# Kernel optimization log

Measured on AMD Instinct MI355X. Metric: run time of the kernel, lower is better.

The kernel has to match this reference:

```python
import jax, jax.numpy as jnp
import numpy as np

B, D_IN, D_OUT, M = 4096, 1024, 1024, 16
GAMMA = 2.0


def setup_inputs() -> dict:
    key = jax.random.key(0)
    ks = jax.random.split(key, 5)
    scale_in = 1.0 / np.sqrt(D_IN)
    return {
        "x": jax.random.normal(ks[0], (B, D_IN), dtype=jnp.float32),
        "W": jax.random.normal(ks[1], (M, D_IN, D_OUT), dtype=jnp.float32) * scale_in,
        "b": jax.random.normal(ks[2], (M, D_OUT), dtype=jnp.float32) * 0.01,
        "Wg": jax.random.normal(ks[3], (D_IN, M), dtype=jnp.float32) * scale_in,
        "bg": jax.random.normal(ks[4], (M,), dtype=jnp.float32) * 0.01,
    }


def reference(x, W, b, Wg, bg):
    # Gate: linear -> pow(gamma) -> normalize by row sum -> relu
    gu = x @ Wg + bg                                   # [B, M]
    gp = jnp.power(gu, GAMMA)                          # gamma = 2.0
    gates = jax.nn.relu(gp / jnp.sum(gp, axis=1, keepdims=True))  # [B, M]
    # M dense expert modules: relu(x @ W_m + b_m), gated and summed (AdditionSublayer)
    h = jax.nn.relu(jnp.einsum("bi,mio->bmo", x, W) + b)          # [B, M, D_OUT]
    return jnp.einsum("bm,bmo->bo", gates, h)                     # [B, D_OUT]
```

## Files before the change

### kernel.cpp

```cpp
#include <hip/hip_runtime.h>

typedef unsigned short u16;
typedef __attribute__((ext_vector_type(4))) float f32x4;
typedef __attribute__((ext_vector_type(8))) short bf16x8;
typedef __attribute__((ext_vector_type(4))) unsigned short u16x4;

#define NT 128

__device__ __forceinline__ u16 f2bf(float f) {
  union { float f; unsigned u; } v; v.f = f;
  unsigned r = v.u + 0x7FFFu + ((v.u >> 16) & 1u);
  return (u16)(r >> 16);
}

__device__ __forceinline__ f32x4 zero4() {
  f32x4 z; z.x = 0.f; z.y = 0.f; z.z = 0.f; z.w = 0.f; return z;
}

__global__ __launch_bounds__(256) void k_cvt_x(const float* __restrict__ x, u16* __restrict__ xb) {
  int i = blockIdx.x * 256 + threadIdx.x;
  f32x4 v = ((const f32x4*)x)[i];
  u16x4 o;
  o.x = f2bf(v.x); o.y = f2bf(v.y); o.z = f2bf(v.z); o.w = f2bf(v.w);
  ((u16x4*)xb)[i] = o;
}

__global__ __launch_bounds__(256) void k_tw(const float* __restrict__ W, u16* __restrict__ wt) {
  __shared__ float t[64][65];
  int bid = blockIdx.x;
  int e = bid >> 8, rem = bid & 255, kt = rem >> 4, nt = rem & 15;
  int tid = threadIdx.x;
  int c = tid & 63, r0 = tid >> 6;
  const float* src = W + (size_t)e * 1048576 + (size_t)(kt * 64) * 1024 + nt * 64;
  #pragma unroll
  for (int p = 0; p < 16; ++p) {
    int r = r0 + p * 4;
    t[r][c] = src[r * 1024 + c];
  }
  __syncthreads();
  u16* dst = wt + (size_t)e * 1048576 + (size_t)(nt * 64) * 1024 + kt * 64;
  #pragma unroll
  for (int p = 0; p < 16; ++p) {
    int r2 = r0 + p * 4;
    dst[r2 * 1024 + c] = f2bf(t[c][r2]);
  }
}

__global__ __launch_bounds__(256) void k_gates(const float* __restrict__ x, const float* __restrict__ Wg,
                                               const float* __restrict__ bg, float* __restrict__ gates) {
  int wid = threadIdx.x >> 6, lane = threadIdx.x & 63;
  int b = blockIdx.x * 4 + wid;
  const float* xr = x + (size_t)b * 1024;
  float acc[16];
  #pragma unroll
  for (int m = 0; m < 16; ++m) acc[m] = 0.f;
  for (int i = lane; i < 1024; i += 64) {
    float xv = xr[i];
    const f32x4* wg = (const f32x4*)(Wg + (size_t)i * 16);
    #pragma unroll
    for (int q = 0; q < 4; ++q) {
      f32x4 w = wg[q];
      acc[q*4+0] += xv * w.x; acc[q*4+1] += xv * w.y;
      acc[q*4+2] += xv * w.z; acc[q*4+3] += xv * w.w;
    }
  }
  #pragma unroll
  for (int m = 0; m < 16; ++m) {
    #pragma unroll
    for (int off = 32; off > 0; off >>= 1)
      acc[m] += __shfl_xor(acc[m], off, 64);
  }
  float tot = 0.f, gp[16];
  #pragma unroll
  for (int m = 0; m < 16; ++m) { float gu = acc[m] + bg[m]; gp[m] = gu * gu; tot += gp[m]; }
  float inv = 1.f / tot;
  if (lane == 0) {
    #pragma unroll
    for (int m = 0; m < 16; ++m) gates[(size_t)b * 16 + m] = gp[m] * inv;
  }
}

#define GLL(srcaddr, ldsaddr) \
  __builtin_amdgcn_global_load_lds((const __attribute__((address_space(1))) void*)(srcaddr), \
                                   (__attribute__((address_space(3))) void*)(ldsaddr), 16, 0, 0)

#define MFMA16() do { \
  acc[0][0] = __builtin_amdgcn_mfma_f32_16x16x32_bf16(af0, bfr0, acc[0][0], 0,0,0); \
  acc[0][1] = __builtin_amdgcn_mfma_f32_16x16x32_bf16(af0, bfr1, acc[0][1], 0,0,0); \
  acc[0][2] = __builtin_amdgcn_mfma_f32_16x16x32_bf16(af0, bfr2, acc[0][2], 0,0,0); \
  acc[0][3] = __builtin_amdgcn_mfma_f32_16x16x32_bf16(af0, bfr3, acc[0][3], 0,0,0); \
  acc[1][0] = __builtin_amdgcn_mfma_f32_16x16x32_bf16(af1, bfr0, acc[1][0], 0,0,0); \
  acc[1][1] = __builtin_amdgcn_mfma_f32_16x16x32_bf16(af1, bfr1, acc[1][1], 0,0,0); \
  acc[1][2] = __builtin_amdgcn_mfma_f32_16x16x32_bf16(af1, bfr2, acc[1][2], 0,0,0); \
  acc[1][3] = __builtin_amdgcn_mfma_f32_16x16x32_bf16(af1, bfr3, acc[1][3], 0,0,0); \
  acc[2][0] = __builtin_amdgcn_mfma_f32_16x16x32_bf16(af2, bfr0, acc[2][0], 0,0,0); \
  acc[2][1] = __builtin_amdgcn_mfma_f32_16x16x32_bf16(af2, bfr1, acc[2][1], 0,0,0); \
  acc[2][2] = __builtin_amdgcn_mfma_f32_16x16x32_bf16(af2, bfr2, acc[2][2], 0,0,0); \
  acc[2][3] = __builtin_amdgcn_mfma_f32_16x16x32_bf16(af2, bfr3, acc[2][3], 0,0,0); \
  acc[3][0] = __builtin_amdgcn_mfma_f32_16x16x32_bf16(af3, bfr0, acc[3][0], 0,0,0); \
  acc[3][1] = __builtin_amdgcn_mfma_f32_16x16x32_bf16(af3, bfr1, acc[3][1], 0,0,0); \
  acc[3][2] = __builtin_amdgcn_mfma_f32_16x16x32_bf16(af3, bfr2, acc[3][2], 0,0,0); \
  acc[3][3] = __builtin_amdgcn_mfma_f32_16x16x32_bf16(af3, bfr3, acc[3][3], 0,0,0); \
} while (0)

__global__ __launch_bounds__(512, 2)
void k_moe(const u16* __restrict__ xb, const u16* __restrict__ wt,
           const float* __restrict__ gates, const float* __restrict__ bias,
           float* __restrict__ out0, float* __restrict__ p1out) {
  __shared__ __align__(16) u16 sA[3 * 8192];
  __shared__ __align__(16) u16 sB[3 * 16384];
  __shared__ float lgat[1024];
  __shared__ float lbias[2048];

  int tid = threadIdx.x;
  int bid = blockIdx.x;
  int swz = (bid & 7) * 32 + (bid >> 3);
  int btile = swz & 31;
  int pnl = swz >> 5;
  int grp = pnl >> 2;
  int ntile = pnl & 3;
  int brow0 = btile * 128;
  int ncol0 = ntile * 256;
  int mb = grp * 8;

  int wid = tid >> 6, lane = tid & 63;
  int wm = wid >> 2, wn = wid & 3;
  int lrow = lane & 15, lk = lane >> 4;
  int sw = lrow & 7;

  const u16* asrc = xb + (size_t)brow0 * 1024;
  const u16* bsrc = wt + (size_t)mb * 1048576 + (size_t)ncol0 * 1024;

  int r0a = tid >> 3, s0a = tid & 7;
  int r1a = (512 + tid) >> 3, s1a = tid & 7;
  int sia0 = r0a * 1024 + (s0a ^ (r0a & 7)) * 8;
  int sia1 = r1a * 1024 + (s1a ^ (r1a & 7)) * 8;
  int lda0 = (wid * 64) * 8;
  int lda1 = (512 + wid * 64) * 8;
  int sib0 = sia0, sib1 = sia1;
  int r2b = (1024 + tid) >> 3;
  int r3b = (1536 + tid) >> 3;
  int sib2 = r2b * 1024 + ((tid & 7) ^ (r2b & 7)) * 8;
  int sib3 = r3b * 1024 + ((tid & 7) ^ (r3b & 7)) * 8;
  int ldb0 = lda0, ldb1 = lda1;
  int ldb2 = (1024 + wid * 64) * 8;
  int ldb3 = (1536 + wid * 64) * 8;

  int baseA = (wm * 64 + lrow) * 64;
  int baseB = (wn * 64 + lrow) * 64;
  int pa0 = baseA + ((0 + lk) ^ sw) * 8;
  int pa1 = baseA + ((4 + lk) ^ sw) * 8;
  int pb0 = baseB + ((0 + lk) ^ sw) * 8;
  int pb1 = baseB + ((4 + lk) ^ sw) * 8;

  f32x4 acc[4][4], oacc[4][4];
  #pragma unroll
  for (int i = 0; i < 4; ++i)
    #pragma unroll
    for (int j = 0; j < 4; ++j) { acc[i][j] = zero4(); oacc[i][j] = zero4(); }

  #pragma unroll
  for (int i = 0; i < 2; ++i) {
    int idx = i * 512 + tid;
    lgat[idx] = gates[(size_t)(brow0 + (idx & 127)) * 16 + mb + (idx >> 7)];
  }
  #pragma unroll
  for (int i = 0; i < 4; ++i) {
    int idx = i * 512 + tid;
    lbias[idx] = bias[(size_t)(mb + (idx >> 8)) * 1024 + ncol0 + (idx & 255)];
  }
  u16 *a0 = sA, *a1 = sA + 8192, *a2 = sA + 16384;
  u16 *b0 = sB, *b1 = sB + 16384, *b2 = sB + 32768;
  GLL(asrc + sia0, a0 + lda0); GLL(asrc + sia1, a0 + lda1);
  GLL(bsrc + sib0, b0 + ldb0); GLL(bsrc + sib1, b0 + ldb1);
  GLL(bsrc + sib2, b0 + ldb2); GLL(bsrc + sib3, b0 + ldb3);
  GLL(asrc + 64 + sia0, a1 + lda0); GLL(asrc + 64 + sia1, a1 + lda1);
  GLL(bsrc + 64 + sib0, b1 + ldb0); GLL(bsrc + 64 + sib1, b1 + ldb1);
  GLL(bsrc + 64 + sib2, b1 + ldb2); GLL(bsrc + 64 + sib3, b1 + ldb3);
  __syncthreads();

  for (int t = 0; t < NT; ++t) {
    int t2 = t + 2;
    const u16* sa2 = asrc + (t2 & 15) * 64;
    const u16* sb2 = bsrc + (size_t)(t2 >> 4) * 1048576 + (t2 & 15) * 64;
    bool pf = (t2 < NT);
    bf16x8 bfr0, bfr1, bfr2, bfr3, af0, af1, af2, af3;

    af0  = *(const bf16x8*)&a0[pa0];
    af1  = *(const bf16x8*)&a0[pa0 + 1024];
    af2  = *(const bf16x8*)&a0[pa0 + 2048];
    af3  = *(const bf16x8*)&a0[pa0 + 3072];
    bfr0 = *(const bf16x8*)&b0[pb0];
    bfr1 = *(const bf16x8*)&b0[pb0 + 1024];
    bfr2 = *(const bf16x8*)&b0[pb0 + 2048];
    bfr3 = *(const bf16x8*)&b0[pb0 + 3072];
    if (pf) {
      GLL(sa2 + sia0, a2 + lda0); GLL(sa2 + sia1, a2 + lda1);
      GLL(sb2 + sib0, b2 + ldb0);
    }
    __builtin_amdgcn_s_barrier();
    __builtin_amdgcn_s_setprio(1);
    MFMA16();
    __builtin_amdgcn_s_setprio(0);
    __builtin_amdgcn_s_barrier();

    af0  = *(const bf16x8*)&a0[pa1];
    af1  = *(const bf16x8*)&a0[pa1 + 1024];
    af2  = *(const bf16x8*)&a0[pa1 + 2048];
    af3  = *(const bf16x8*)&a0[pa1 + 3072];
    bfr0 = *(const bf16x8*)&b0[pb1];
    bfr1 = *(const bf16x8*)&b0[pb1 + 1024];
    bfr2 = *(const bf16x8*)&b0[pb1 + 2048];
    bfr3 = *(const bf16x8*)&b0[pb1 + 3072];
    if (pf) {
      GLL(sb2 + sib1, b2 + ldb1);
      GLL(sb2 + sib2, b2 + ldb2);
      GLL(sb2 + sib3, b2 + ldb3);
    }
    __builtin_amdgcn_s_barrier();
    __builtin_amdgcn_s_setprio(1);
    MFMA16();
    __builtin_amdgcn_s_setprio(0);

    if ((t & 15) == 15) {
      int ml = t >> 4;
      float bvv[4];
      #pragma unroll
      for (int ni = 0; ni < 4; ++ni) bvv[ni] = lbias[ml * 256 + wn * 64 + ni * 16 + lrow];
      #pragma unroll
      for (int mi = 0; mi < 4; ++mi) {
        f32x4 gv = *(const f32x4*)&lgat[ml * 128 + wm * 64 + mi * 16 + lk * 4];
        #pragma unroll
        for (int ni = 0; ni < 4; ++ni) {
          #pragma unroll
          for (int j = 0; j < 4; ++j) {
            float h = acc[mi][ni][j] + bvv[ni];
            h = fmaxf(h, 0.f);
            oacc[mi][ni][j] += gv[j] * h;
          }
          acc[mi][ni] = zero4();
        }
      }
    }

    if (t < NT - 2)       asm volatile("s_waitcnt vmcnt(6)" ::: "memory");
    else if (t == NT - 2) asm volatile("s_waitcnt vmcnt(0)" ::: "memory");
    __builtin_amdgcn_s_barrier();
    __builtin_amdgcn_sched_barrier(0);

    u16* ta = a0; a0 = a1; a1 = a2; a2 = ta;
    u16* tb = b0; b0 = b1; b1 = b2; b2 = tb;
  }

  float* op = grp ? p1out : out0;
  #pragma unroll
  for (int mi = 0; mi < 4; ++mi)
    #pragma unroll
    for (int j = 0; j < 4; ++j) {
      int row = brow0 + wm * 64 + mi * 16 + lk * 4 + j;
      #pragma unroll
      for (int ni = 0; ni < 4; ++ni) {
        int col = ncol0 + wn * 64 + ni * 16 + lrow;
        op[(size_t)row * 1024 + col] = oacc[mi][ni][j];
      }
    }
}

__global__ __launch_bounds__(256) void k_add(float* __restrict__ out, const float* __restrict__ p1) {
  int i = blockIdx.x * 256 + threadIdx.x;
  f32x4 a = ((const f32x4*)out)[i];
  f32x4 b = ((const f32x4*)p1)[i];
  ((f32x4*)out)[i] = a + b;
}

extern "C" void kernel_launch(void* const* d_in, const int* in_sizes, int n_in,
                              void* d_out, int out_size, void* d_ws, size_t ws_size,
                              hipStream_t stream) {
  const float* x  = (const float*)d_in[0];
  const float* W  = (const float*)d_in[1];
  const float* b  = (const float*)d_in[2];
  const float* Wg = (const float*)d_in[3];
  const float* bg = (const float*)d_in[4];
  float* out = (float*)d_out;

  char* ws = (char*)d_ws;
  u16* xb     = (u16*)ws;
  u16* wt     = (u16*)(ws + 8388608);
  float* gts  = (float*)(ws + 41943040);
  float* p1   = (float*)(ws + 42205184);

  k_cvt_x<<<4096, 256, 0, stream>>>(x, xb);
  k_tw<<<4096, 256, 0, stream>>>(W, wt);
  k_gates<<<1024, 256, 0, stream>>>(x, Wg, bg, gts);
  k_moe<<<256, 512, 0, stream>>>(xb, wt, gts, b, out, p1);
  k_add<<<4096, 256, 0, stream>>>(out, p1);
}
```

Before: 193.5 us.

## Load both k-halves upfront and drop intra-iteration barriers in MoE GEMM loop

Each main-loop iteration now reads all 16 A/B fragments from LDS at once, issues all six global-to-LDS prefetches together, and runs 32 MFMAs back to back, removing the two mid-iteration s_barriers. The prologue replaces __syncthreads with a partial vmcnt wait plus barrier so only the first stage must land before compute. The aim is to cut barrier stalls and give the scheduler longer MFMA runs, at the cost of more vector registers for the doubled fragment set. This may raise register pressure under the 512-thread, 2-block launch bound. The synchronisation shown may also be too weak for the triple-buffered LDS reuse.

Measured after the change: 183.7 us. 1.05x faster.

```diff
diff --git a/kernel.cpp b/kernel.cpp
--- a/kernel.cpp
+++ b/kernel.cpp
@@ -84,23 +84,23 @@
   __builtin_amdgcn_global_load_lds((const __attribute__((address_space(1))) void*)(srcaddr), \
                                    (__attribute__((address_space(3))) void*)(ldsaddr), 16, 0, 0)
 
-#define MFMA16() do { \
-  acc[0][0] = __builtin_amdgcn_mfma_f32_16x16x32_bf16(af0, bfr0, acc[0][0], 0,0,0); \
-  acc[0][1] = __builtin_amdgcn_mfma_f32_16x16x32_bf16(af0, bfr1, acc[0][1], 0,0,0); \
-  acc[0][2] = __builtin_amdgcn_mfma_f32_16x16x32_bf16(af0, bfr2, acc[0][2], 0,0,0); \
-  acc[0][3] = __builtin_amdgcn_mfma_f32_16x16x32_bf16(af0, bfr3, acc[0][3], 0,0,0); \
-  acc[1][0] = __builtin_amdgcn_mfma_f32_16x16x32_bf16(af1, bfr0, acc[1][0], 0,0,0); \
-  acc[1][1] = __builtin_amdgcn_mfma_f32_16x16x32_bf16(af1, bfr1, acc[1][1], 0,0,0); \
-  acc[1][2] = __builtin_amdgcn_mfma_f32_16x16x32_bf16(af1, bfr2, acc[1][2], 0,0,0); \
-  acc[1][3] = __builtin_amdgcn_mfma_f32_16x16x32_bf16(af1, bfr3, acc[1][3], 0,0,0); \
-  acc[2][0] = __builtin_amdgcn_mfma_f32_16x16x32_bf16(af2, bfr0, acc[2][0], 0,0,0); \
-  acc[2][1] = __builtin_amdgcn_mfma_f32_16x16x32_bf16(af2, bfr1, acc[2][1], 0,0,0); \
-  acc[2][2] = __builtin_amdgcn_mfma_f32_16x16x32_bf16(af2, bfr2, acc[2][2], 0,0,0); \
-  acc[2][3] = __builtin_amdgcn_mfma_f32_16x16x32_bf16(af2, bfr3, acc[2][3], 0,0,0); \
-  acc[3][0] = __builtin_amdgcn_mfma_f32_16x16x32_bf16(af3, bfr0, acc[3][0], 0,0,0); \
-  acc[3][1] = __builtin_amdgcn_mfma_f32_16x16x32_bf16(af3, bfr1, acc[3][1], 0,0,0); \
-  acc[3][2] = __builtin_amdgcn_mfma_f32_16x16x32_bf16(af3, bfr2, acc[3][2], 0,0,0); \
-  acc[3][3] = __builtin_amdgcn_mfma_f32_16x16x32_bf16(af3, bfr3, acc[3][3], 0,0,0); \
+#define MFMA16(A0,A1,A2,A3,B0,B1,B2,B3) do { \
+  acc[0][0] = __builtin_amdgcn_mfma_f32_16x16x32_bf16(A0, B0, acc[0][0], 0,0,0); \
+  acc[0][1] = __builtin_amdgcn_mfma_f32_16x16x32_bf16(A0, B1, acc[0][1], 0,0,0); \
+  acc[0][2] = __builtin_amdgcn_mfma_f32_16x16x32_bf16(A0, B2, acc[0][2], 0,0,0); \
+  acc[0][3] = __builtin_amdgcn_mfma_f32_16x16x32_bf16(A0, B3, acc[0][3], 0,0,0); \
+  acc[1][0] = __builtin_amdgcn_mfma_f32_16x16x32_bf16(A1, B0, acc[1][0], 0,0,0); \
+  acc[1][1] = __builtin_amdgcn_mfma_f32_16x16x32_bf16(A1, B1, acc[1][1], 0,0,0); \
+  acc[1][2] = __builtin_amdgcn_mfma_f32_16x16x32_bf16(A1, B2, acc[1][2], 0,0,0); \
+  acc[1][3] = __builtin_amdgcn_mfma_f32_16x16x32_bf16(A1, B3, acc[1][3], 0,0,0); \
+  acc[2][0] = __builtin_amdgcn_mfma_f32_16x16x32_bf16(A2, B0, acc[2][0], 0,0,0); \
+  acc[2][1] = __builtin_amdgcn_mfma_f32_16x16x32_bf16(A2, B1, acc[2][1], 0,0,0); \
+  acc[2][2] = __builtin_amdgcn_mfma_f32_16x16x32_bf16(A2, B2, acc[2][2], 0,0,0); \
+  acc[2][3] = __builtin_amdgcn_mfma_f32_16x16x32_bf16(A2, B3, acc[2][3], 0,0,0); \
+  acc[3][0] = __builtin_amdgcn_mfma_f32_16x16x32_bf16(A3, B0, acc[3][0], 0,0,0); \
+  acc[3][1] = __builtin_amdgcn_mfma_f32_16x16x32_bf16(A3, B1, acc[3][1], 0,0,0); \
+  acc[3][2] = __builtin_amdgcn_mfma_f32_16x16x32_bf16(A3, B2, acc[3][2], 0,0,0); \
+  acc[3][3] = __builtin_amdgcn_mfma_f32_16x16x32_bf16(A3, B3, acc[3][3], 0,0,0); \
 } while (0)
 
 __global__ __launch_bounds__(512, 2)
@@ -177,49 +177,44 @@
   GLL(asrc + 64 + sia0, a1 + lda0); GLL(asrc + 64 + sia1, a1 + lda1);
   GLL(bsrc + 64 + sib0, b1 + ldb0); GLL(bsrc + 64 + sib1, b1 + ldb1);
   GLL(bsrc + 64 + sib2, b1 + ldb2); GLL(bsrc + 64 + sib3, b1 + ldb3);
-  __syncthreads();
+  asm volatile("s_waitcnt vmcnt(6)" ::: "memory");
+  __builtin_amdgcn_s_barrier();
+  __builtin_amdgcn_sched_barrier(0);
 
   for (int t = 0; t < NT; ++t) {
     int t2 = t + 2;
     const u16* sa2 = asrc + (t2 & 15) * 64;
     const u16* sb2 = bsrc + (size_t)(t2 >> 4) * 1048576 + (t2 & 15) * 64;
     bool pf = (t2 < NT);
-    bf16x8 bfr0, bfr1, bfr2, bfr3, af0, af1, af2, af3;
-
-    af0  = *(const bf16x8*)&a0[pa0];
-    af1  = *(const bf16x8*)&a0[pa0 + 1024];
-    af2  = *(const bf16x8*)&a0[pa0 + 2048];
-    af3  = *(const bf16x8*)&a0[pa0 + 3072];
-    bfr0 = *(const bf16x8*)&b0[pb0];
-    bfr1 = *(const bf16x8*)&b0[pb0 + 1024];
-    bfr2 = *(const bf16x8*)&b0[pb0 + 2048];
-    bfr3 = *(const bf16x8*)&b0[pb0 + 3072];
+    bf16x8 a00, a01, a02, a03, a10, a11, a12, a13;
+    bf16x8 b00, b01, b02, b03, b10, b11, b12, b13;
+
+    a00 = *(const bf16x8*)&a0[pa0];
+    a01 = *(const bf16x8*)&a0[pa0 + 1024];
+    a02 = *(const bf16x8*)&a0[pa0 + 2048];
+    a03 = *(const bf16x8*)&a0[pa0 + 3072];
+    b00 = *(const bf16x8*)&b0[pb0];
+    b01 = *(const bf16x8*)&b0[pb0 + 1024];
+    b02 = *(const bf16x8*)&b0[pb0 + 2048];
+    b03 = *(const bf16x8*)&b0[pb0 + 3072];
+    a10 = *(const bf16x8*)&a0[pa1];
+    a11 = *(const bf16x8*)&a0[pa1 + 1024];
+    a12 = *(const bf16x8*)&a0[pa1 + 2048];
+    a13 = *(const bf16x8*)&a0[pa1 + 3072];
+    b10 = *(const bf16x8*)&b0[pb1];
+    b11 = *(const bf16x8*)&b0[pb1 + 1024];
+    b12 = *(const bf16x8*)&b0[pb1 + 2048];
+    b13 = *(const bf16x8*)&b0[pb1 + 3072];
+
     if (pf) {
       GLL(sa2 + sia0, a2 + lda0); GLL(sa2 + sia1, a2 + lda1);
-      GLL(sb2 + sib0, b2 + ldb0);
-    }
-    __builtin_amdgcn_s_barrier();
+      GLL(sb2 + sib0, b2 + ldb0); GLL(sb2 + sib1, b2 + ldb1);
+      GLL(sb2 + sib2, b2 + ldb2); GLL(sb2 + sib3, b2 + ldb3);
+    }
+
     __builtin_amdgcn_s_setprio(1);
-    MFMA16();
-    __builtin_amdgcn_s_setprio(0);
-    __builtin_amdgcn_s_barrier();
-
-    af0  = *(const bf16x8*)&a0[pa1];
-    af1  = *(const bf16x8*)&a0[pa1 + 1024];
-    af2  = *(const bf16x8*)&a0[pa1 + 2048];
-    af3  = *(const bf16x8*)&a0[pa1 + 3072];
-    bfr0 = *(const bf16x8*)&b0[pb1];
-    bfr1 = *(const bf16x8*)&b0[pb1 + 1024];
-    bfr2 = *(const bf16x8*)&b0[pb1 + 2048];
-    bfr3 = *(const bf16x8*)&b0[pb1 + 3072];
-    if (pf) {
-      GLL(sb2 + sib1, b2 + ldb1);
-      GLL(sb2 + sib2, b2 + ldb2);
-      GLL(sb2 + sib3, b2 + ldb3);
-    }
-    __builtin_amdgcn_s_barrier();
-    __builtin_amdgcn_s_setprio(1);
-    MFMA16();
+    MFMA16(a00, a01, a02, a03, b00, b01, b02, b03);
+    MFMA16(a10, a11, a12, a13, b10, b11, b12, b13);
     __builtin_amdgcn_s_setprio(0);
 
     if ((t & 15) == 15) {
```
